# Kernel optimization log

Measured on AMD Instinct MI355X. Metric: run time of the kernel, lower is better.

Reference implementation:

```python
import jax, jax.numpy as jnp
import numpy as np

B, S, T = 256, 2048, 64


def setup_inputs() -> dict:
    key = jax.random.key(0)
    k1, k2, k3, k4, k5 = jax.random.split(key, 5)
    emissions = jax.random.normal(k1, (B, S, T), dtype=jnp.float32)
    tags = jax.random.randint(k2, (B, S), 0, T)
    mask = jnp.ones((B, S), dtype=jnp.int32)
    start_transitions = jax.random.uniform(k3, (T,), minval=-1.0, maxval=1.0, dtype=jnp.float32)
    end_transitions = jax.random.uniform(k4, (T,), minval=-1.0, maxval=1.0, dtype=jnp.float32)
    transitions = jax.random.uniform(k5, (T, T), minval=-1.0, maxval=1.0, dtype=jnp.float32)
    return {
        'emissions': emissions,
        'start_transitions': start_transitions,
        'end_transitions': end_transitions,
        'transitions': transitions,
        'tags': tags,
        'mask': mask,
    }


def _crf_nll(emissions, start_transitions, end_transitions, transitions, tags, mask):
    # batch_first=True -> convert to time-major like the torch code
    em = jnp.swapaxes(emissions, 0, 1)            # (S, B, T)
    tg = tags.T                                   # (S, B)
    mk = mask.T.astype(emissions.dtype)           # (S, B)
    barange = jnp.arange(em.shape[1])

    # ---- numerator: score of the gold tag path ----
    score0 = start_transitions[tg[0]] + em[0, barange, tg[0]]  # (B,)

    def num_step(score, inp):
        em_i, tg_prev, tg_i, m_i = inp
        score = score + (transitions[tg_prev, tg_i] + em_i[barange, tg_i]) * m_i
        return score, None

    numerator, _ = jax.lax.scan(num_step, score0, (em[1:], tg[:-1], tg[1:], mk[1:]))
    seq_ends = mk.sum(axis=0).astype(jnp.int32) - 1            # (B,)
    last_tags = tg[seq_ends, barange]
    numerator = numerator + end_transitions[last_tags]

    # ---- denominator: log partition via forward algorithm (log-sum-exp semiring) ----
    alpha0 = start_transitions + em[0]                          # (B, T)

    def den_step(alpha, inp):
        em_i, m_i = inp
        # (B, T_prev, T_next) broadcast-add, reduce over T_prev
        nxt = jax.nn.logsumexp(alpha[:, :, None] + transitions[None, :, :] + em_i[:, None, :], axis=1)
        alpha = jnp.where(m_i[:, None] > 0, nxt, alpha)
        return alpha, None

    alpha, _ = jax.lax.scan(den_step, alpha0, (em[1:], mk[1:]))
    denominator = jax.nn.logsumexp(alpha + end_transitions, axis=1)  # (B,)

    return -(numerator - denominator).mean()


def reference(emissions, start_transitions, end_transitions, transitions, tags, mask):
    return _crf_nll(emissions, start_transitions, end_transitions, transitions, tags, mask)
```

## Files before the change

### kernel.cpp

```cpp
#include <hip/hip_runtime.h>

#define BB 256
#define SS 2048
#define TT 64
#define KC 16
#define LC (SS / KC)
#define WARM 48

typedef __fp16 half2v __attribute__((ext_vector_type(2)));
typedef __fp16 half8v __attribute__((ext_vector_type(8)));

__device__ __forceinline__ float rfl_f(float x) {
  return __builtin_bit_cast(float, __builtin_amdgcn_readfirstlane(__builtin_bit_cast(int, x)));
}

__device__ __forceinline__ void crf_step(float& q, int& esum, float x,
                                         const half2v (&E2)[32],
                                         __fp16* qsh, int j) {
  const half8v* qv = (const half8v*)qsh;
  half2v a0 = (half2v)0, a1 = (half2v)0, a2 = (half2v)0, a3 = (half2v)0;
#pragma unroll
  for (int m = 0; m < 8; ++m) {
    half8v blk = qv[m];
    a0 += __builtin_shufflevector(blk, blk, 0, 1) * E2[4 * m + 0];
    a1 += __builtin_shufflevector(blk, blk, 2, 3) * E2[4 * m + 1];
    a2 += __builtin_shufflevector(blk, blk, 4, 5) * E2[4 * m + 2];
    a3 += __builtin_shufflevector(blk, blk, 6, 7) * E2[4 * m + 3];
  }
  half2v s = (a0 + a1) + (a2 + a3);
  float y = (float)s[0] + (float)s[1];
  float t = y * x;
  float v = rfl_f(t);
  int eb = __builtin_bit_cast(int, v) & 0x7f800000;
  float scale = __builtin_bit_cast(float, 0x7C000000 - eb);
  q = t * scale;
  esum += (eb >> 23);
  qsh[j] = (__fp16)q;
}

__device__ __forceinline__ void prefetch8(float (&buf)[8], int& mreg, float& tvg,
                                          float& evg, int i0, bool gather,
                                          const float* __restrict__ ep,
                                          const float* __restrict__ emb,
                                          const int* __restrict__ mp,
                                          const int* __restrict__ tg,
                                          const float* __restrict__ trans, int j) {
#pragma unroll
  for (int t = 0; t < 8; ++t) {
    int ii = i0 + t;
    ii = ii > SS - 1 ? SS - 1 : ii;
    ii = ii < 0 ? 0 : ii;
    buf[t] = ep[ii * TT];
  }
  int mi = i0 + (j & 7);
  int mc = mi > SS - 1 ? SS - 1 : mi;
  mc = mc < 1 ? 1 : mc;
  mreg = (mi > SS - 1 || mi < 1) ? 0 : mp[mc];
  tvg = 0.f;
  evg = 0.f;
  if (gather && j < 8) {
    int tgc = tg[mc];
    int tgp = tg[mc - 1];
    tvg = trans[tgp * TT + tgc];
    evg = emb[(size_t)mc * TT + tgc];
  }
}

__device__ __forceinline__ void process8(float& q, int& esum, int& nsteps,
                                         const float (&buf)[8], int mreg,
                                         const half2v (&E2)[32], __fp16* qsh, int j) {
  unsigned long long bal = __ballot(mreg != 0);
  if (bal == ~0ull) {
    float xs[8];
#pragma unroll
    for (int t = 0; t < 8; ++t) xs[t] = __expf(buf[t]);
#pragma unroll
    for (int t = 0; t < 8; ++t) crf_step(q, esum, xs[t], E2, qsh, j);
    nsteps += 8;
  } else if (bal != 0ull) {
#pragma unroll
    for (int t = 0; t < 8; ++t) {
      int mv = __builtin_amdgcn_readlane(mreg, t);
      if (mv) {
        crf_step(q, esum, __expf(buf[t]), E2, qsh, j);
        nsteps += 1;
      }
    }
  }
}

__global__ __launch_bounds__(64, 4) void crf_kernel(
    const float* __restrict__ em, const float* __restrict__ startT,
    const float* __restrict__ endT, const float* __restrict__ trans,
    const int* __restrict__ tags, const int* __restrict__ mask,
    float* __restrict__ out) {
  __shared__ alignas(16) __fp16 qsh[TT];
  const int b = blockIdx.x >> 4;
  const int c = blockIdx.x & (KC - 1);
  const int j = threadIdx.x;

  half2v E2[32];
#pragma unroll
  for (int m = 0; m < 32; ++m) {
    float e0 = __expf(trans[(2 * m) * TT + j]) * 0.03125f;
    float e1 = __expf(trans[(2 * m + 1) * TT + j]) * 0.03125f;
    E2[m] = __builtin_amdgcn_cvt_pkrtz(e0, e1);
  }

  const float* emb = em + (size_t)b * SS * TT;
  const float* ep = emb + j;
  const int* mp = mask + b * SS;
  const int* tg = tags + b * SS;

  float q, gamma_c0 = 0.f, pnum = 0.f;
  if (c == 0) {
    float a0v = startT[j] + ep[0];
    float a00 = rfl_f(a0v);
    q = __expf(a0v - a00) * 0.015625f;
    gamma_c0 = a00 * 1.4426950408889634f;
    int tg0 = tg[0];
    if (j == 0) pnum = startT[tg0] + emb[tg0];
  } else {
    q = 0.015625f;
  }
  qsh[j] = (__fp16)q;
  int esum = 0, nsteps = 0, nsteps0 = 0;
  float sS = 0.f;

  const int base = c * LC - WARM + 1;
  const int t0 = (c == 0) ? 6 : 0;

  float bufA[8], bufB[8];
  int mA, mB;
  float tvA, evA, tvB, evB;
  prefetch8(bufA, mA, tvA, evA, base + 8 * t0, t0 >= 6, ep, emb, mp, tg, trans, j);
  for (int t = t0; t < 22; t += 2) {
    prefetch8(bufB, mB, tvB, evB, base + 8 * (t + 1), t + 1 >= 6, ep, emb, mp, tg, trans, j);
    if (t == 6 && c != 0) {
      sS = __log2f(rfl_f(q)) + (float)(6 + esum - 116 * nsteps);
      nsteps0 = nsteps;
    }
    process8(q, esum, nsteps, bufA, mA, E2, qsh, j);
    pnum += (mA != 0) ? (tvA + evA) : 0.f;
    prefetch8(bufA, mA, tvA, evA, base + 8 * (t + 2), t + 2 >= 6, ep, emb, mp, tg, trans, j);
    process8(q, esum, nsteps, bufB, mB, E2, qsh, j);
    pnum += (mB != 0) ? (tvB + evB) : 0.f;
  }

  float v_end = rfl_f(q);
  float eS = __log2f(v_end) + (float)(6 + esum - 116 * nsteps) + gamma_c0;
  float contrib = 0.69314718055994531f * (eS - sS);

  if (c == KC - 1) {
    float arel = 0.69314718055994531f * (__log2f(q) - __log2f(v_end)) + endT[j];
    float mx = arel;
#pragma unroll
    for (int o = 32; o > 0; o >>= 1) mx = fmaxf(mx, __shfl_xor(mx, o, 64));
    float ex = __expf(arel - mx);
#pragma unroll
    for (int o = 32; o > 0; o >>= 1) ex += __shfl_xor(ex, o, 64);
    contrib += mx + __logf(ex);
    int lastTag = tg[c * LC + (nsteps - nsteps0)];
    contrib -= endT[lastTag];
  }

  float nsum = pnum;
#pragma unroll
  for (int o = 32; o > 0; o >>= 1) nsum += __shfl_xor(nsum, o, 64);

  if (j == 0) atomicAdd(out, (contrib - nsum) * (1.0f / BB));
}

extern "C" void kernel_launch(void* const* d_in, const int* in_sizes, int n_in,
                              void* d_out, int out_size, void* d_ws, size_t ws_size,
                              hipStream_t stream) {
  const float* em = (const float*)d_in[0];
  const float* startT = (const float*)d_in[1];
  const float* endT = (const float*)d_in[2];
  const float* trans = (const float*)d_in[3];
  const int* tags = (const int*)d_in[4];
  const int* mask = (const int*)d_in[5];
  float* out = (float*)d_out;

  (void)hipMemsetAsync(out, 0, sizeof(float), stream);
  crf_kernel<<<BB * KC, 64, 0, stream>>>(em, startT, endT, trans, tags, mask, out);
}
```

Measured before the change: 263.6 us.

## Double sequence chunks, pack two waves per block, use fdot2, spread atomics

Splits each sequence into 32 chunks instead of 16, so every wave does a shorter serial recurrence. Two chunk-waves now share a 128-thread block. The half2 multiply-accumulate is replaced with fdot2 instructions that accumulate in fp32. The single-address atomic is spread across 128 padded workspace slots, followed by a small reduce kernel. The aim is more parallelism and a shorter serial chain per wave, less atomic contention, and better dot-product precision. The costs are relatively more warm-up recomputation per chunk and an extra kernel launch and memset.

```diff
diff --git a/kernel.cpp b/kernel.cpp
--- a/kernel.cpp
+++ b/kernel.cpp
@@ -3,9 +3,13 @@
 #define BB 256
 #define SS 2048
 #define TT 64
-#define KC 16
+#define KC 32
 #define LC (SS / KC)
 #define WARM 48
+#define W8 (WARM / 8)
+#define TBLK ((WARM + LC) / 8)
+#define NSLOT 128
+#define SLOT_STRIDE 32
 
 typedef __fp16 half2v __attribute__((ext_vector_type(2)));
 typedef __fp16 half8v __attribute__((ext_vector_type(8)));
@@ -18,6 +22,18 @@
                                          const half2v (&E2)[32],
                                          __fp16* qsh, int j) {
   const half8v* qv = (const half8v*)qsh;
+#if __has_builtin(__builtin_amdgcn_fdot2)
+  float d0 = 0.f, d1 = 0.f, d2 = 0.f, d3 = 0.f;
+#pragma unroll
+  for (int m = 0; m < 8; ++m) {
+    half8v blk = qv[m];
+    d0 = __builtin_amdgcn_fdot2(__builtin_shufflevector(blk, blk, 0, 1), E2[4 * m + 0], d0, false);
+    d1 = __builtin_amdgcn_fdot2(__builtin_shufflevector(blk, blk, 2, 3), E2[4 * m + 1], d1, false);
+    d2 = __builtin_amdgcn_fdot2(__builtin_shufflevector(blk, blk, 4, 5), E2[4 * m + 2], d2, false);
+    d3 = __builtin_amdgcn_fdot2(__builtin_shufflevector(blk, blk, 6, 7), E2[4 * m + 3], d3, false);
+  }
+  float y = (d0 + d1) + (d2 + d3);
+#else
   half2v a0 = (half2v)0, a1 = (half2v)0, a2 = (half2v)0, a3 = (half2v)0;
 #pragma unroll
   for (int m = 0; m < 8; ++m) {
@@ -29,6 +45,7 @@
   }
   half2v s = (a0 + a1) + (a2 + a3);
   float y = (float)s[0] + (float)s[1];
+#endif
   float t = y * x;
   float v = rfl_f(t);
   int eb = __builtin_bit_cast(int, v) & 0x7f800000;
@@ -89,15 +106,18 @@
   }
 }
 
-__global__ __launch_bounds__(64, 4) void crf_kernel(
+__global__ __launch_bounds__(128, 8) void crf_kernel(
     const float* __restrict__ em, const float* __restrict__ startT,
     const float* __restrict__ endT, const float* __restrict__ trans,
     const int* __restrict__ tags, const int* __restrict__ mask,
-    float* __restrict__ out) {
-  __shared__ alignas(16) __fp16 qsh[TT];
-  const int b = blockIdx.x >> 4;
-  const int c = blockIdx.x & (KC - 1);
-  const int j = threadIdx.x;
+    float* __restrict__ acc, int slotmask) {
+  __shared__ alignas(16) __fp16 qsh2[2][TT];
+  const int wid = threadIdx.x >> 6;
+  const int j = threadIdx.x & 63;
+  const int sid = (blockIdx.x << 1) | wid;
+  const int b = sid >> 5;
+  const int c = sid & (KC - 1);
+  __fp16* qsh = qsh2[wid];
 
   half2v E2[32];
 #pragma unroll
@@ -128,21 +148,21 @@
   float sS = 0.f;
 
   const int base = c * LC - WARM + 1;
-  const int t0 = (c == 0) ? 6 : 0;
+  const int t0 = (c == 0) ? W8 : 0;
 
   float bufA[8], bufB[8];
   int mA, mB;
   float tvA, evA, tvB, evB;
-  prefetch8(bufA, mA, tvA, evA, base + 8 * t0, t0 >= 6, ep, emb, mp, tg, trans, j);
-  for (int t = t0; t < 22; t += 2) {
-    prefetch8(bufB, mB, tvB, evB, base + 8 * (t + 1), t + 1 >= 6, ep, emb, mp, tg, trans, j);
-    if (t == 6 && c != 0) {
+  prefetch8(bufA, mA, tvA, evA, base + 8 * t0, t0 >= W8, ep, emb, mp, tg, trans, j);
+  for (int t = t0; t < TBLK; t += 2) {
+    prefetch8(bufB, mB, tvB, evB, base + 8 * (t + 1), t + 1 >= W8, ep, emb, mp, tg, trans, j);
+    if (t == W8 && c != 0) {
       sS = __log2f(rfl_f(q)) + (float)(6 + esum - 116 * nsteps);
       nsteps0 = nsteps;
     }
     process8(q, esum, nsteps, bufA, mA, E2, qsh, j);
     pnum += (mA != 0) ? (tvA + evA) : 0.f;
-    prefetch8(bufA, mA, tvA, evA, base + 8 * (t + 2), t + 2 >= 6, ep, emb, mp, tg, trans, j);
+    prefetch8(bufA, mA, tvA, evA, base + 8 * (t + 2), t + 2 >= W8, ep, emb, mp, tg, trans, j);
     process8(q, esum, nsteps, bufB, mB, E2, qsh, j);
     pnum += (mB != 0) ? (tvB + evB) : 0.f;
   }
@@ -168,7 +188,18 @@
 #pragma unroll
   for (int o = 32; o > 0; o >>= 1) nsum += __shfl_xor(nsum, o, 64);
 
-  if (j == 0) atomicAdd(out, (contrib - nsum) * (1.0f / BB));
+  if (j == 0)
+    atomicAdd(acc + (size_t)(sid & slotmask) * SLOT_STRIDE,
+              (contrib - nsum) * (1.0f / BB));
+}
+
+__global__ __launch_bounds__(64) void reduce_kernel(const float* __restrict__ ws,
+                                                    float* __restrict__ out) {
+  float v = ws[(size_t)threadIdx.x * SLOT_STRIDE] +
+            ws[(size_t)(threadIdx.x + 64) * SLOT_STRIDE];
+#pragma unroll
+  for (int o = 32; o > 0; o >>= 1) v += __shfl_xor(v, o, 64);
+  if (threadIdx.x == 0) *out = v;
 }
 
 extern "C" void kernel_launch(void* const* d_in, const int* in_sizes, int n_in,
@@ -182,6 +213,15 @@
   const int* mask = (const int*)d_in[5];
   float* out = (float*)d_out;
 
-  (void)hipMemsetAsync(out, 0, sizeof(float), stream);
-  crf_kernel<<<BB * KC, 64, 0, stream>>>(em, startT, endT, trans, tags, mask, out);
-}
+  const size_t need = (size_t)NSLOT * SLOT_STRIDE * sizeof(float);
+  if (d_ws && ws_size >= need) {
+    (void)hipMemsetAsync(d_ws, 0, need, stream);
+    crf_kernel<<<BB * KC / 2, 128, 0, stream>>>(em, startT, endT, trans, tags,
+                                                mask, (float*)d_ws, NSLOT - 1);
+    reduce_kernel<<<1, 64, 0, stream>>>((const float*)d_ws, out);
+  } else {
+    (void)hipMemsetAsync(out, 0, sizeof(float), stream);
+    crf_kernel<<<BB * KC / 2, 128, 0, stream>>>(em, startT, endT, trans, tags,
+                                                mask, out, 0);
+  }
+}
```

Result: slower. 413.0 us (+56.6%).
